# Kernel optimization log

Measured on AMD Instinct MI355X. Metric: run time of the kernel, lower is better.

## Reference

```python
import jax, jax.numpy as jnp
import numpy as np

N = 30000       # nodes
E = 480000      # edges (before self-loops)
G = 64          # graphs in batch
IN = 128        # in_channels
HID = 128       # hidden_dim
HEADS = 4
NEG_SLOPE = 0.2


def gat_layer(x, src, dst, W, att_src, att_dst, b):
    """PyG-style GATConv: W [Fin, H*C], att_* [H, C], b [H*C]. Returns [N, H*C] (head concat)."""
    H, C = att_src.shape
    h = (x @ W).reshape(-1, H, C)                      # [N, H, C]
    a_s = jnp.einsum('nhc,hc->nh', h, att_src)         # [N, H]
    a_d = jnp.einsum('nhc,hc->nh', h, att_dst)
    e = jax.nn.leaky_relu(a_s[src] + a_d[dst], NEG_SLOPE)   # [Etot, H]
    # segment softmax over edges grouped by destination node
    m = jax.ops.segment_max(e, dst, num_segments=N)
    e = jnp.exp(e - m[dst])
    denom = jax.ops.segment_sum(e, dst, num_segments=N)
    alpha = e / (denom[dst] + 1e-16)                   # [Etot, H]
    msg = h[src] * alpha[:, :, None]                   # [Etot, H, C]
    out = jax.ops.segment_sum(msg, dst, num_segments=N)
    return out.reshape(-1, H * C) + b


def setup_inputs():
    key = jax.random.key(0)
    ks = jax.random.split(key, 13)
    s = 0.05
    x = jax.random.normal(ks[0], (N, IN), jnp.float32)
    edge_index = jax.random.randint(ks[1], (2, E), 0, N, dtype=jnp.int32)
    batch = jnp.sort(jax.random.randint(ks[2], (N,), 0, G, dtype=jnp.int32))
    return {
        'x': x,
        'edge_index': edge_index,
        'batch': batch,
        'W1': jax.random.normal(ks[3], (IN, HEADS * HID), jnp.float32) * s,
        'att_src1': jax.random.normal(ks[4], (HEADS, HID), jnp.float32) * s,
        'att_dst1': jax.random.normal(ks[5], (HEADS, HID), jnp.float32) * s,
        'b1': jnp.zeros((HEADS * HID,), jnp.float32),
        'W2': jax.random.normal(ks[6], (HEADS * HID, HID), jnp.float32) * s,
        'att_src2': jax.random.normal(ks[7], (1, HID), jnp.float32) * s,
        'att_dst2': jax.random.normal(ks[8], (1, HID), jnp.float32) * s,
        'b2': jnp.zeros((HID,), jnp.float32),
        'lin_w': jax.random.normal(ks[9], (HID, 1), jnp.float32) * s,
        'lin_b': jnp.zeros((1,), jnp.float32),
    }


def reference(x, edge_index, batch, W1, att_src1, att_dst1, b1, W2, att_src2, att_dst2, b2, lin_w, lin_b):
    # add self-loops (PyG GATConv default)
    loop = jnp.arange(N, dtype=edge_index.dtype)
    src = jnp.concatenate([edge_index[0], loop])
    dst = jnp.concatenate([edge_index[1], loop])

    h = gat_layer(x, src, dst, W1, att_src1, att_dst1, b1)   # [N, 4*HID]
    h = jax.nn.elu(h)
    h = gat_layer(h, src, dst, W2, att_src2, att_dst2, b2)   # [N, HID]
    h = jax.nn.elu(h)

    # global mean pool over graphs
    sums = jax.ops.segment_sum(h, batch, num_segments=G)     # [G, HID]
    cnts = jax.ops.segment_sum(jnp.ones((N,), h.dtype), batch, num_segments=G)
    pooled = sums / jnp.maximum(cnts, 1.0)[:, None]

    out = pooled @ lin_w + lin_b                             # [G, 1]
    return out.squeeze(-1)                                   # [G]
```

## Files before the change

### kernel.cpp

```cpp
#include <hip/hip_runtime.h>

#define NN    30000
#define EE    480000
#define ETOT  (EE + NN)
#define GG    64
#define IN_CH 128
#define HID   128
#define HEADS 4
#define F1    (HEADS * HID)
#define CAP   64

typedef __attribute__((ext_vector_type(8))) __bf16 bf16x8;
typedef __attribute__((ext_vector_type(4))) float  floatx4;
typedef __attribute__((ext_vector_type(2))) float  f32x2;

__device__ __forceinline__ float lrelu(float x) { return x > 0.f ? x : 0.2f * x; }
__device__ __forceinline__ float elu_f(float x) { return x > 0.f ? x : (expf(x) - 1.f); }
__device__ __forceinline__ unsigned short f2bf(float f) {
    unsigned int u = __float_as_uint(f);
    return (unsigned short)((u + 0x7FFFu + ((u >> 16) & 1u)) >> 16);
}
__device__ __forceinline__ float bf2f(unsigned short u) {
    return __uint_as_float(((unsigned int)u) << 16);
}
__device__ __forceinline__ f32x2 fma2(float a, f32x2 v, f32x2 acc) {
    f32x2 av = {a, a};
    return __builtin_elementwise_fma(av, v, acc);
}

#define LDKC 136
__global__ __launch_bounds__(256) void gemm_bf16(const unsigned short* __restrict__ A, int lda, int zA,
                                                 const unsigned short* __restrict__ Bt, int zBt, int K,
                                                 unsigned short* __restrict__ C, int ldc, int zC,
                                                 const float* __restrict__ bias, int zBias,
                                                 int M, int do_elu,
                                                 const float* __restrict__ ws,
                                                 const float* __restrict__ wd,
                                                 float* __restrict__ as_out,
                                                 float* __restrict__ ad_out)
{
    A  += (size_t)blockIdx.z * zA;
    Bt += (size_t)blockIdx.z * zBt;
    C  += (size_t)blockIdx.z * zC;
    const float* bias_p = bias ? bias + (size_t)blockIdx.z * zBias : nullptr;

    __shared__ unsigned short Bl[128 * LDKC];

    const int tid  = threadIdx.x;
    const int wave = tid >> 6, lane = tid & 63;
    const int quad = lane >> 4, l16 = lane & 15;
    const int bm = blockIdx.x * 128;

    floatx4 zf = {0.f, 0.f, 0.f, 0.f};
    floatx4 acc[2][8];
#pragma unroll
    for (int rt = 0; rt < 2; rt++)
#pragma unroll
        for (int ct = 0; ct < 8; ct++) acc[rt][ct] = zf;

    float bb[8];
#pragma unroll
    for (int ct = 0; ct < 8; ct++) bb[ct] = bias_p ? bias_p[ct * 16 + l16] : 0.f;

    const int r0 = bm + wave * 32 + l16;
    const int r1 = r0 + 16;

    for (int kc = 0; kc < K; kc += 128) {
        uint4 av[2][4];
#pragma unroll
        for (int kb = 0; kb < 4; kb++) {
            const int k = kc + kb * 32 + quad * 8;
            av[0][kb] = (r0 < M) ? *(const uint4*)(A + (size_t)r0 * lda + k) : uint4{0,0,0,0};
            av[1][kb] = (r1 < M) ? *(const uint4*)(A + (size_t)r1 * lda + k) : uint4{0,0,0,0};
        }

        if (kc) __syncthreads();
#pragma unroll
        for (int i = 0; i < 8; i++) {
            int j = i * 256 + tid;
            int n = j >> 4, ko = (j & 15) * 8;
            *(uint4*)&Bl[n * LDKC + ko] = *(const uint4*)(Bt + (size_t)n * K + kc + ko);
        }
        __syncthreads();

#pragma unroll
        for (int kb = 0; kb < 4; kb++) {
            bf16x8 bfr[8];
#pragma unroll
            for (int ct = 0; ct < 8; ct++)
                bfr[ct] = *(bf16x8*)&Bl[(ct * 16 + l16) * LDKC + kb * 32 + quad * 8];
            bf16x8 a0 = *(bf16x8*)&av[0][kb];
            bf16x8 a1 = *(bf16x8*)&av[1][kb];
#pragma unroll
            for (int ct = 0; ct < 8; ct++) {
                acc[0][ct] = __builtin_amdgcn_mfma_f32_16x16x32_bf16(a0, bfr[ct], acc[0][ct], 0, 0, 0);
                acc[1][ct] = __builtin_amdgcn_mfma_f32_16x16x32_bf16(a1, bfr[ct], acc[1][ct], 0, 0, 0);
            }
        }
    }

    __syncthreads();
    unsigned short* wls = Bl + wave * (16 * 128);
#pragma unroll
    for (int rt = 0; rt < 2; rt++) {
        if (rt) __builtin_amdgcn_wave_barrier();
#pragma unroll
        for (int ct = 0; ct < 8; ct++) {
#pragma unroll
            for (int reg = 0; reg < 4; reg++) {
                float v = acc[rt][ct][reg] + bb[ct];
                if (do_elu) v = elu_f(v);
                wls[(quad * 4 + reg) * 128 + ct * 16 + l16] = f2bf(v);
            }
        }
        __builtin_amdgcn_wave_barrier();
#pragma unroll
        for (int i = 0; i < 4; i++) {
            int j = i * 64 + lane;
            int rl = j >> 4, off = (j & 15) * 8;
            int row = bm + wave * 32 + rt * 16 + rl;
            if (row < M)
                *(uint4*)(C + (size_t)row * ldc + off) = *(uint4*)&wls[rl * 128 + off];
        }
        if (ws) {
            int row = bm + wave * 32 + rt * 16 + l16;
            const unsigned short* rowp = &wls[l16 * 128 + quad * 32];
            float ps = 0.f, pd = 0.f;
#pragma unroll
            for (int jj = 0; jj < 32; jj++) {
                float hv = bf2f(rowp[jj]);
                ps = fmaf(hv, ws[quad * 32 + jj], ps);
                pd = fmaf(hv, wd[quad * 32 + jj], pd);
            }
            ps += __shfl_xor(ps, 16); ps += __shfl_xor(ps, 32);
            pd += __shfl_xor(pd, 16); pd += __shfl_xor(pd, 32);
            if (quad == 0 && row < M) { as_out[row] = ps; ad_out[row] = pd; }
        }
    }
}

__global__ void prep_k(const float* __restrict__ W1, const float* __restrict__ W2,
                       const float* __restrict__ att_s, const float* __restrict__ att_d,
                       unsigned short* __restrict__ W1t, unsigned short* __restrict__ W2t,
                       float* __restrict__ wt, int* __restrict__ deg,
                       float* __restrict__ pooled_cnt)
{
    int b = blockIdx.x;
    if (b < 256) {
        int idx = b * 256 + threadIdx.x;
        int h = idx >> 14, rem = idx & 16383, n = rem >> 7, k = rem & 127;
        W1t[idx] = f2bf(W1[(size_t)k * F1 + h * 128 + n]);
    } else if (b < 512) {
        int idx = (b - 256) * 256 + threadIdx.x;
        int n = idx >> 9, k = idx & 511;
        W2t[idx] = f2bf(W2[(size_t)k * HID + n]);
    } else if (b < 520) {
        if (threadIdx.x < 128) {
            int q = b - 512;
            int h = q & 3, sd = q >> 2;
            int i = threadIdx.x;
            const float* att = (sd ? att_d : att_s) + h * 128;
            const float* wr = W1 + (size_t)i * F1 + h * 128;
            float acc = 0.f;
            for (int c = 0; c < 128; c++) acc = fmaf(wr[c], att[c], acc);
            wt[sd * 512 + h * 128 + i] = acc;
        }
    } else if (b < 638) {
        int i = (b - 520) * 256 + threadIdx.x;
        if (i < NN) deg[i] = 0;
    } else {
        int i = (b - 638) * 256 + threadIdx.x;
        if (i < GG * HID + GG) pooled_cnt[i] = 0.f;
    }
}

#define SCORE_BLKS ((NN + 31) / 32)
__global__ __launch_bounds__(256) void scorefill_k(const float* __restrict__ x,
                                                   const float* __restrict__ wt,
                                                   float* __restrict__ a_s,
                                                   float* __restrict__ a_d,
                                                   unsigned short* __restrict__ x16,
                                                   const int* __restrict__ ei,
                                                   int* __restrict__ deg,
                                                   int* __restrict__ perm)
{
    int b = blockIdx.x;
    int t = threadIdx.x;
    if (b < SCORE_BLKS) {
        __shared__ __align__(16) float swt[1024];
        ((float4*)swt)[t] = ((const float4*)wt)[t];
        __syncthreads();
        const int node0 = b * 32;
        int node = node0 + (t >> 3);
        int q = t & 7;
        int h = q & 3, sd = q >> 2;
        if (node < NN) {
            const float4* xr = (const float4*)(x + (size_t)node * IN_CH);
            const float4* wr = (const float4*)(swt + sd * 512 + h * 128);
            float acc = 0.f;
#pragma unroll 4
            for (int c = 0; c < 32; c++) {
                float4 xv = xr[c], wv = wr[c];
                acc = fmaf(xv.x, wv.x, acc);
                acc = fmaf(xv.y, wv.y, acc);
                acc = fmaf(xv.z, wv.z, acc);
                acc = fmaf(xv.w, wv.w, acc);
            }
            if (sd == 0) a_s[node * 4 + h] = acc;
            else         a_d[node * 4 + h] = acc;
        }
        int col = t & 127;
#pragma unroll 4
        for (int r = (t >> 7); r < 32; r += 2) {
            int nr = node0 + r;
            if (nr < NN)
                x16[(size_t)nr * IN_CH + col] = f2bf(x[(size_t)nr * IN_CH + col]);
        }
    } else {
        int i = (b - SCORE_BLKS) * 256 + t;
        if (i < ETOT) {
            int s, d;
            if (i < EE) { s = ei[i]; d = ei[EE + i]; }
            else        { s = i - EE; d = i - EE; }
            int p = atomicAdd(&deg[d], 1);
            if (p < CAP) perm[(size_t)d * CAP + p] = s;
        }
    }
}

__global__ __launch_bounds__(256) void gat_agg1w(const unsigned short* __restrict__ x16,
                                                 const float* __restrict__ a_s,
                                                 const float* __restrict__ a_d,
                                                 const int* __restrict__ deg,
                                                 const int* __restrict__ perm,
                                                 unsigned short* __restrict__ agg)
{
    __shared__ int    sSrc[4][64];
    __shared__ __align__(16) float4 sE[4][64];
    const int wave = threadIdx.x >> 6;
    const int lane = threadIdx.x & 63;
    const int hw   = lane >> 5;
    const int c4   = (lane & 31) * 4;
    int n = blockIdx.x * 4 + wave;
    if (n >= NN) return;
    const int rem = min(deg[n], CAP);
    const float4 ad4 = *(const float4*)(a_d + (size_t)n * 4);

    if (lane < rem) {
        int sj = perm[(size_t)n * CAP + lane];
        float4 av = *(const float4*)(a_s + (size_t)sj * 4);
        sSrc[wave][lane] = sj;
        sE[wave][lane] = make_float4(__expf(lrelu(av.x + ad4.x)), __expf(lrelu(av.y + ad4.y)),
                                     __expf(lrelu(av.z + ad4.z)), __expf(lrelu(av.w + ad4.w)));
    }
    __builtin_amdgcn_wave_barrier();

    f32x2 aLo[4] = {{0,0},{0,0},{0,0},{0,0}};
    f32x2 aHi[4] = {{0,0},{0,0},{0,0},{0,0}};
    f32x2 den01 = {0,0}, den23 = {0,0};

    for (int j = hw; j < rem; j += 2) {
        int s = sSrc[wave][j];
        float4 ev = sE[wave][j];
        den01 += (f32x2){ev.x, ev.y};
        den23 += (f32x2){ev.z, ev.w};
        uint2 uv = *(const uint2*)(x16 + (size_t)s * IN_CH + c4);
        f32x2 xlo = { __uint_as_float(uv.x << 16), __uint_as_float(uv.x & 0xFFFF0000u) };
        f32x2 xhi = { __uint_as_float(uv.y << 16), __uint_as_float(uv.y & 0xFFFF0000u) };
        aLo[0] = fma2(ev.x, xlo, aLo[0]); aHi[0] = fma2(ev.x, xhi, aHi[0]);
        aLo[1] = fma2(ev.y, xlo, aLo[1]); aHi[1] = fma2(ev.y, xhi, aHi[1]);
        aLo[2] = fma2(ev.z, xlo, aLo[2]); aHi[2] = fma2(ev.z, xhi, aHi[2]);
        aLo[3] = fma2(ev.w, xlo, aLo[3]); aHi[3] = fma2(ev.w, xhi, aHi[3]);
    }
#pragma unroll
    for (int h = 0; h < 4; h++) {
        aLo[h].x += __shfl_xor(aLo[h].x, 32); aLo[h].y += __shfl_xor(aLo[h].y, 32);
        aHi[h].x += __shfl_xor(aHi[h].x, 32); aHi[h].y += __shfl_xor(aHi[h].y, 32);
    }
    den01.x += __shfl_xor(den01.x, 32); den01.y += __shfl_xor(den01.y, 32);
    den23.x += __shfl_xor(den23.x, 32); den23.y += __shfl_xor(den23.y, 32);
    const float iv0 = 1.f / (den01.x + 1e-16f), iv1 = 1.f / (den01.y + 1e-16f);
    const float iv2 = 1.f / (den23.x + 1e-16f), iv3 = 1.f / (den23.y + 1e-16f);

#pragma unroll
    for (int k = 0; k < 2; k++) {
        int h = hw * 2 + k;
        f32x2 lo = hw ? aLo[2 + k] : aLo[k];
        f32x2 hi = hw ? aHi[2 + k] : aHi[k];
        float iv = hw ? (k ? iv3 : iv2) : (k ? iv1 : iv0);
        uint2 o;
        o.x = (unsigned)f2bf(lo.x * iv) | ((unsigned)f2bf(lo.y * iv) << 16);
        o.y = (unsigned)f2bf(hi.x * iv) | ((unsigned)f2bf(hi.y * iv) << 16);
        *(uint2*)(agg + (size_t)n * F1 + h * 128 + c4) = o;
    }
}

__global__ __launch_bounds__(256) void gat_agg2w(const unsigned short* __restrict__ h16,
                                                 const float* __restrict__ a_s,
                                                 const float* __restrict__ a_d,
                                                 const int* __restrict__ deg,
                                                 const int* __restrict__ perm,
                                                 const float* __restrict__ bias,
                                                 unsigned short* __restrict__ out16)
{
    int n = blockIdx.x * 4 + (threadIdx.x >> 6);
    if (n >= NN) return;
    const int lane = threadIdx.x & 63;
    const int hw   = lane >> 5;
    const int c4   = (lane & 31) * 4;
    const int rem = min(deg[n], CAP);
    const float ad = a_d[n];

    int sj = 0; float e = 0.f;
    if (lane < rem) {
        sj = perm[(size_t)n * CAP + lane];
        e = __expf(lrelu(a_s[sj] + ad));
    }
    f32x2 accLo = {0,0}, accHi = {0,0};
    float den = 0.f;
    for (int j = hw; j < rem; j += 2) {
        int   s = __shfl(sj, j);
        float a = __shfl(e, j);
        den += a;
        uint2 uv = *(const uint2*)(h16 + (size_t)s * HID + c4);
        f32x2 lo = { __uint_as_float(uv.x << 16), __uint_as_float(uv.x & 0xFFFF0000u) };
        f32x2 hi = { __uint_as_float(uv.y << 16), __uint_as_float(uv.y & 0xFFFF0000u) };
        accLo = fma2(a, lo, accLo);
        accHi = fma2(a, hi, accHi);
    }
    accLo.x += __shfl_xor(accLo.x, 32); accLo.y += __shfl_xor(accLo.y, 32);
    accHi.x += __shfl_xor(accHi.x, 32); accHi.y += __shfl_xor(accHi.y, 32);
    den += __shfl_xor(den, 32);
    const float inv = 1.f / (den + 1e-16f);
    if (hw == 0) {
        float4 bb = *(const float4*)(bias + c4);
        uint2 o;
        o.x = (unsigned)f2bf(elu_f(accLo.x * inv + bb.x)) |
              ((unsigned)f2bf(elu_f(accLo.y * inv + bb.y)) << 16);
        o.y = (unsigned)f2bf(elu_f(accHi.x * inv + bb.z)) |
              ((unsigned)f2bf(elu_f(accHi.y * inv + bb.w)) << 16);
        *(uint2*)(out16 + (size_t)n * HID + c4) = o;
    }
}

#define NPB 64
__global__ __launch_bounds__(128) void pool_seg_k(const unsigned short* __restrict__ out16,
                                                  const int* __restrict__ batch,
                                                  float* __restrict__ pooled,
                                                  float* __restrict__ cnt)
{
    int n0 = blockIdx.x * NPB;
    int n1 = min(n0 + NPB, NN);
    if (n0 >= n1) return;
    int t = threadIdx.x;
    int cur = batch[n0];
    float acc = 0.f;
    int count = 0;
    for (int n = n0; n < n1; n++) {
        int g = batch[n];
        if (g != cur) {
            atomicAdd(&pooled[cur * HID + t], acc);
            if (t == 0) atomicAdd(&cnt[cur], (float)count);
            acc = 0.f; count = 0; cur = g;
        }
        acc += bf2f(out16[(size_t)n * HID + t]);
        count++;
    }
    atomicAdd(&pooled[cur * HID + t], acc);
    if (t == 0) atomicAdd(&cnt[cur], (float)count);
}

__global__ void final_k(const float* __restrict__ pooled, const float* __restrict__ cnt,
                        const float* __restrict__ lw, const float* __restrict__ lb,
                        float* __restrict__ outp)
{
    int g = threadIdx.x;
    if (g < GG) {
        float acc = 0.f;
        for (int c = 0; c < HID; c++) acc += pooled[g * HID + c] * lw[c];
        float cc = fmaxf(cnt[g], 1.0f);
        outp[g] = acc / cc + lb[0];
    }
}

extern "C" void kernel_launch(void* const* d_in, const int* in_sizes, int n_in,
                              void* d_out, int out_size, void* d_ws, size_t ws_size,
                              hipStream_t stream)
{
    const float* x    = (const float*)d_in[0];
    const int*   ei   = (const int*)d_in[1];
    const int*   batch= (const int*)d_in[2];
    const float* W1   = (const float*)d_in[3];
    const float* as1w = (const float*)d_in[4];
    const float* ad1w = (const float*)d_in[5];
    const float* b1   = (const float*)d_in[6];
    const float* W2   = (const float*)d_in[7];
    const float* as2w = (const float*)d_in[8];
    const float* ad2w = (const float*)d_in[9];
    const float* b2   = (const float*)d_in[10];
    const float* lw   = (const float*)d_in[11];
    const float* lb   = (const float*)d_in[12];
    float* outp = (float*)d_out;

    char* w = (char*)d_ws;
    size_t off = 0;
    auto alloc = [&](size_t bytes) -> char* {
        char* p = w + off;
        off += (bytes + 255) & ~(size_t)255;
        return p;
    };
    char*  reg0   = alloc((size_t)NN * F1 * 4);
    char*  reg1   = alloc((size_t)NN * F1 * 2);
    unsigned short* x16 = (unsigned short*)alloc((size_t)NN * IN_CH * 2);
    unsigned short* W1t = (unsigned short*)alloc(65536 * 2);
    unsigned short* W2t = (unsigned short*)alloc(65536 * 2);
    float* wt1    = (float*)alloc(1024 * 4);
    float* a_s1   = (float*)alloc((size_t)NN * 4 * 4);
    float* a_d1   = (float*)alloc((size_t)NN * 4 * 4);
    float* a_s2   = (float*)alloc((size_t)NN * 4);
    float* a_d2   = (float*)alloc((size_t)NN * 4);
    int*   deg    = (int*)alloc((size_t)NN * 4);
    int*   perm   = (int*)alloc((size_t)NN * CAP * 4);
    float* pooled = (float*)alloc((size_t)(GG * HID + GG) * 4);
    float* cnt    = pooled + GG * HID;

    unsigned short* agg16   = (unsigned short*)reg0;
    unsigned short* out116  = (unsigned short*)reg1;
    unsigned short* hh2_16  = (unsigned short*)reg0;
    unsigned short* out2_16 = (unsigned short*)reg0 + (size_t)NN * HID;

    prep_k<<<671, 256, 0, stream>>>(W1, W2, as1w, ad1w, W1t, W2t, wt1, deg, pooled);

    const int FILL_BLKS = (ETOT + 255) / 256;
    scorefill_k<<<SCORE_BLKS + FILL_BLKS, 256, 0, stream>>>(x, wt1, a_s1, a_d1, x16,
                                                            ei, deg, perm);

    gat_agg1w<<<(NN + 3) / 4, 256, 0, stream>>>(x16, a_s1, a_d1, deg, perm, agg16);
    const int MT = (NN + 127) / 128;
    gemm_bf16<<<dim3(MT, 1, 4), 256, 0, stream>>>(agg16, F1, 128, W1t, 128 * 128, 128,
                                                  out116, F1, 128, b1, 128, NN, 1,
                                                  nullptr, nullptr, nullptr, nullptr);

    gemm_bf16<<<dim3(MT, 1, 1), 256, 0, stream>>>(out116, F1, 0, W2t, 0, F1,
                                                  hh2_16, HID, 0, nullptr, 0, NN, 0,
                                                  as2w, ad2w, a_s2, a_d2);
    gat_agg2w<<<(NN + 3) / 4, 256, 0, stream>>>(hh2_16, a_s2, a_d2, deg, perm, b2, out2_16);

    pool_seg_k<<<(NN + NPB - 1) / NPB, 128, 0, stream>>>(out2_16, batch, pooled, cnt);
    final_k<<<1, 64, 0, stream>>>(pooled, cnt, lw, lb, outp);
}
```

Baseline: 239.5 us.

## Fuse layer-1 projection GEMM with layer-2 GEMM per 32-row tile

Replaces the two separate GEMM launches (layer-1 per-head projection with bias+ELU, then layer-2 projection with attention scores) with one kernel. Each block processes 32 rows, computes each head's 128-column slice of the layer-1 output into shared memory, and immediately accumulates it into the layer-2 result. This removes the write and re-read of the NN×512 bf16 intermediate and one kernel launch. In exchange, W1/W2 tiles are reloaded into LDS for every 32-row block rather than every 128-row block, and each block runs with smaller MFMA tiles and more barriers.

```diff
diff --git a/kernel.cpp b/kernel.cpp
--- a/kernel.cpp
+++ b/kernel.cpp
@@ -28,114 +28,142 @@
     return __builtin_elementwise_fma(av, v, acc);
 }
 
-#define LDKC 136
-__global__ __launch_bounds__(256) void gemm_bf16(const unsigned short* __restrict__ A, int lda, int zA,
-                                                 const unsigned short* __restrict__ Bt, int zBt, int K,
-                                                 unsigned short* __restrict__ C, int ldc, int zC,
-                                                 const float* __restrict__ bias, int zBias,
-                                                 int M, int do_elu,
-                                                 const float* __restrict__ ws,
-                                                 const float* __restrict__ wd,
-                                                 float* __restrict__ as_out,
-                                                 float* __restrict__ ad_out)
-{
-    A  += (size_t)blockIdx.z * zA;
-    Bt += (size_t)blockIdx.z * zBt;
-    C  += (size_t)blockIdx.z * zC;
-    const float* bias_p = bias ? bias + (size_t)blockIdx.z * zBias : nullptr;
-
-    __shared__ unsigned short Bl[128 * LDKC];
+#define LDW 136
+__global__ __launch_bounds__(256) void gemm12_k(const unsigned short* __restrict__ agg,
+                                                const unsigned short* __restrict__ W1t,
+                                                const unsigned short* __restrict__ W2t,
+                                                const float* __restrict__ b1,
+                                                unsigned short* __restrict__ hh2,
+                                                const float* __restrict__ ws,
+                                                const float* __restrict__ wd,
+                                                float* __restrict__ as_out,
+                                                float* __restrict__ ad_out,
+                                                int M)
+{
+    __shared__ unsigned short Bl[128 * LDW];
+    __shared__ unsigned short H1c[32 * LDW];
 
     const int tid  = threadIdx.x;
-    const int wave = tid >> 6, lane = tid & 63;
+    const int w    = tid >> 6, lane = tid & 63;
     const int quad = lane >> 4, l16 = lane & 15;
-    const int bm = blockIdx.x * 128;
+    const int bm   = blockIdx.x * 32;
 
     floatx4 zf = {0.f, 0.f, 0.f, 0.f};
-    floatx4 acc[2][8];
+    floatx4 acc2[2][2];
 #pragma unroll
     for (int rt = 0; rt < 2; rt++)
 #pragma unroll
-        for (int ct = 0; ct < 8; ct++) acc[rt][ct] = zf;
-
-    float bb[8];
-#pragma unroll
-    for (int ct = 0; ct < 8; ct++) bb[ct] = bias_p ? bias_p[ct * 16 + l16] : 0.f;
-
-    const int r0 = bm + wave * 32 + l16;
-    const int r1 = r0 + 16;
-
-    for (int kc = 0; kc < K; kc += 128) {
+        for (int ct = 0; ct < 2; ct++) acc2[rt][ct] = zf;
+
+    for (int h = 0; h < 4; h++) {
         uint4 av[2][4];
 #pragma unroll
-        for (int kb = 0; kb < 4; kb++) {
-            const int k = kc + kb * 32 + quad * 8;
-            av[0][kb] = (r0 < M) ? *(const uint4*)(A + (size_t)r0 * lda + k) : uint4{0,0,0,0};
-            av[1][kb] = (r1 < M) ? *(const uint4*)(A + (size_t)r1 * lda + k) : uint4{0,0,0,0};
-        }
-
-        if (kc) __syncthreads();
+        for (int rt = 0; rt < 2; rt++) {
+            int r = bm + rt * 16 + l16;
+#pragma unroll
+            for (int kb = 0; kb < 4; kb++)
+                av[rt][kb] = (r < M)
+                    ? *(const uint4*)(agg + (size_t)r * F1 + h * 128 + kb * 32 + quad * 8)
+                    : uint4{0, 0, 0, 0};
+        }
+
+        __syncthreads();
 #pragma unroll
         for (int i = 0; i < 8; i++) {
             int j = i * 256 + tid;
             int n = j >> 4, ko = (j & 15) * 8;
-            *(uint4*)&Bl[n * LDKC + ko] = *(const uint4*)(Bt + (size_t)n * K + kc + ko);
+            *(uint4*)&Bl[n * LDW + ko] = *(const uint4*)(W1t + h * 16384 + n * 128 + ko);
         }
         __syncthreads();
 
+        floatx4 acc1[2][2];
+#pragma unroll
+        for (int rt = 0; rt < 2; rt++)
+#pragma unroll
+            for (int ct = 0; ct < 2; ct++) acc1[rt][ct] = zf;
 #pragma unroll
         for (int kb = 0; kb < 4; kb++) {
-            bf16x8 bfr[8];
-#pragma unroll
-            for (int ct = 0; ct < 8; ct++)
-                bfr[ct] = *(bf16x8*)&Bl[(ct * 16 + l16) * LDKC + kb * 32 + quad * 8];
-            bf16x8 a0 = *(bf16x8*)&av[0][kb];
-            bf16x8 a1 = *(bf16x8*)&av[1][kb];
-#pragma unroll
-            for (int ct = 0; ct < 8; ct++) {
-                acc[0][ct] = __builtin_amdgcn_mfma_f32_16x16x32_bf16(a0, bfr[ct], acc[0][ct], 0, 0, 0);
-                acc[1][ct] = __builtin_amdgcn_mfma_f32_16x16x32_bf16(a1, bfr[ct], acc[1][ct], 0, 0, 0);
+            bf16x8 bfr[2];
+#pragma unroll
+            for (int ct = 0; ct < 2; ct++)
+                bfr[ct] = *(bf16x8*)&Bl[(w * 32 + ct * 16 + l16) * LDW + kb * 32 + quad * 8];
+#pragma unroll
+            for (int rt = 0; rt < 2; rt++) {
+                bf16x8 a = *(bf16x8*)&av[rt][kb];
+#pragma unroll
+                for (int ct = 0; ct < 2; ct++)
+                    acc1[rt][ct] = __builtin_amdgcn_mfma_f32_16x16x32_bf16(a, bfr[ct], acc1[rt][ct], 0, 0, 0);
             }
         }
+
+        float bb[2] = { b1[h * 128 + w * 32 + l16], b1[h * 128 + w * 32 + 16 + l16] };
+#pragma unroll
+        for (int rt = 0; rt < 2; rt++)
+#pragma unroll
+            for (int ct = 0; ct < 2; ct++)
+#pragma unroll
+                for (int reg = 0; reg < 4; reg++) {
+                    float v = elu_f(acc1[rt][ct][reg] + bb[ct]);
+                    H1c[(rt * 16 + quad * 4 + reg) * LDW + w * 32 + ct * 16 + l16] = f2bf(v);
+                }
+        __syncthreads();
+#pragma unroll
+        for (int i = 0; i < 8; i++) {
+            int j = i * 256 + tid;
+            int n = j >> 4, ko = (j & 15) * 8;
+            *(uint4*)&Bl[n * LDW + ko] = *(const uint4*)(W2t + (size_t)n * F1 + h * 128 + ko);
+        }
+        __syncthreads();
+
+#pragma unroll
+        for (int kb = 0; kb < 4; kb++) {
+            bf16x8 af[2], bfr[2];
+#pragma unroll
+            for (int rt = 0; rt < 2; rt++)
+                af[rt] = *(bf16x8*)&H1c[(rt * 16 + l16) * LDW + kb * 32 + quad * 8];
+#pragma unroll
+            for (int ct = 0; ct < 2; ct++)
+                bfr[ct] = *(bf16x8*)&Bl[(w * 32 + ct * 16 + l16) * LDW + kb * 32 + quad * 8];
+#pragma unroll
+            for (int rt = 0; rt < 2; rt++)
+#pragma unroll
+                for (int ct = 0; ct < 2; ct++)
+                    acc2[rt][ct] = __builtin_amdgcn_mfma_f32_16x16x32_bf16(af[rt], bfr[ct], acc2[rt][ct], 0, 0, 0);
+        }
     }
 
     __syncthreads();
-    unsigned short* wls = Bl + wave * (16 * 128);
-#pragma unroll
-    for (int rt = 0; rt < 2; rt++) {
-        if (rt) __builtin_amdgcn_wave_barrier();
-#pragma unroll
-        for (int ct = 0; ct < 8; ct++) {
-#pragma unroll
-            for (int reg = 0; reg < 4; reg++) {
-                float v = acc[rt][ct][reg] + bb[ct];
-                if (do_elu) v = elu_f(v);
-                wls[(quad * 4 + reg) * 128 + ct * 16 + l16] = f2bf(v);
-            }
-        }
-        __builtin_amdgcn_wave_barrier();
-#pragma unroll
-        for (int i = 0; i < 4; i++) {
-            int j = i * 64 + lane;
-            int rl = j >> 4, off = (j & 15) * 8;
-            int row = bm + wave * 32 + rt * 16 + rl;
-            if (row < M)
-                *(uint4*)(C + (size_t)row * ldc + off) = *(uint4*)&wls[rl * 128 + off];
-        }
-        if (ws) {
-            int row = bm + wave * 32 + rt * 16 + l16;
-            const unsigned short* rowp = &wls[l16 * 128 + quad * 32];
-            float ps = 0.f, pd = 0.f;
-#pragma unroll
-            for (int jj = 0; jj < 32; jj++) {
-                float hv = bf2f(rowp[jj]);
-                ps = fmaf(hv, ws[quad * 32 + jj], ps);
-                pd = fmaf(hv, wd[quad * 32 + jj], pd);
-            }
-            ps += __shfl_xor(ps, 16); ps += __shfl_xor(ps, 32);
-            pd += __shfl_xor(pd, 16); pd += __shfl_xor(pd, 32);
-            if (quad == 0 && row < M) { as_out[row] = ps; ad_out[row] = pd; }
-        }
+#pragma unroll
+    for (int rt = 0; rt < 2; rt++)
+#pragma unroll
+        for (int ct = 0; ct < 2; ct++)
+#pragma unroll
+            for (int reg = 0; reg < 4; reg++)
+                Bl[(rt * 16 + quad * 4 + reg) * 128 + w * 32 + ct * 16 + l16] =
+                    f2bf(acc2[rt][ct][reg]);
+    __syncthreads();
+#pragma unroll
+    for (int i = 0; i < 2; i++) {
+        int j = i * 256 + tid;
+        int rl = j >> 4, off = (j & 15) * 8;
+        int row = bm + rl;
+        if (row < M)
+            *(uint4*)(hh2 + (size_t)row * HID + off) = *(uint4*)&Bl[rl * 128 + off];
+    }
+    if (w < 2) {
+        int rl = w * 16 + l16;
+        int row = bm + rl;
+        const unsigned short* rowp = &Bl[rl * 128 + quad * 32];
+        float ps = 0.f, pd = 0.f;
+#pragma unroll
+        for (int jj = 0; jj < 32; jj++) {
+            float hv = bf2f(rowp[jj]);
+            ps = fmaf(hv, ws[quad * 32 + jj], ps);
+            pd = fmaf(hv, wd[quad * 32 + jj], pd);
+        }
+        ps += __shfl_xor(ps, 16); ps += __shfl_xor(ps, 32);
+        pd += __shfl_xor(pd, 16); pd += __shfl_xor(pd, 32);
+        if (quad == 0 && row < M) { as_out[row] = ps; ad_out[row] = pd; }
     }
 }
 
@@ -409,8 +437,8 @@
         off += (bytes + 255) & ~(size_t)255;
         return p;
     };
-    char*  reg0   = alloc((size_t)NN * F1 * 4);
-    char*  reg1   = alloc((size_t)NN * F1 * 2);
+    char*  reg0   = alloc((size_t)NN * F1 * 2);
+    char*  reg1   = alloc((size_t)NN * HID * 2 * 2);
     unsigned short* x16 = (unsigned short*)alloc((size_t)NN * IN_CH * 2);
     unsigned short* W1t = (unsigned short*)alloc(65536 * 2);
     unsigned short* W2t = (unsigned short*)alloc(65536 * 2);
@@ -425,9 +453,8 @@
     float* cnt    = pooled + GG * HID;
 
     unsigned short* agg16   = (unsigned short*)reg0;
-    unsigned short* out116  = (unsigned short*)reg1;
-    unsigned short* hh2_16  = (unsigned short*)reg0;
-    unsigned short* out2_16 = (unsigned short*)reg0 + (size_t)NN * HID;
+    unsigned short* hh2_16  = (unsigned short*)reg1;
+    unsigned short* out2_16 = (unsigned short*)reg1 + (size_t)NN * HID;
 
     prep_k<<<671, 256, 0, stream>>>(W1, W2, as1w, ad1w, W1t, W2t, wt1, deg, pooled);
 
@@ -436,14 +463,10 @@
                                                             ei, deg, perm);
 
     gat_agg1w<<<(NN + 3) / 4, 256, 0, stream>>>(x16, a_s1, a_d1, deg, perm, agg16);
-    const int MT = (NN + 127) / 128;
-    gemm_bf16<<<dim3(MT, 1, 4), 256, 0, stream>>>(agg16, F1, 128, W1t, 128 * 128, 128,
-                                                  out116, F1, 128, b1, 128, NN, 1,
-                                                  nullptr, nullptr, nullptr, nullptr);
-
-    gemm_bf16<<<dim3(MT, 1, 1), 256, 0, stream>>>(out116, F1, 0, W2t, 0, F1,
-                                                  hh2_16, HID, 0, nullptr, 0, NN, 0,
-                                                  as2w, ad2w, a_s2, a_d2);
+
+    gemm12_k<<<(NN + 31) / 32, 256, 0, stream>>>(agg16, W1t, W2t, b1, hh2_16,
+                                                 as2w, ad2w, a_s2, a_d2, NN);
+
     gat_agg2w<<<(NN + 3) / 4, 256, 0, stream>>>(hh2_16, a_s2, a_d2, deg, perm, b2, out2_16);
 
     pool_seg_k<<<(NN + NPB - 1) / NPB, 128, 0, stream>>>(out2_16, batch, pooled, cnt);
```

Result: no change. 236.2 us (median of 3 runs) (-1.4%).
